# Performance work log

Measured on AMD Instinct MI355X. Metric: run time of the kernel, lower is better.

Reference implementation:

```python
import jax, jax.numpy as jnp
import numpy as np

B, L, D = 2, 1024, 1024
H = 16
NL = 2
DFF = 4 * D
EPS = 1e-5
W_SCALE = 0.02


def rmsnorm(x, w):
    # x * rsqrt(mean(x^2, -1) + eps) * w   (computed in fp32 as in the torch code)
    xf = x.astype(jnp.float32)
    n = xf * jax.lax.rsqrt(jnp.mean(xf * xf, axis=-1, keepdims=True) + EPS)
    return n.astype(x.dtype) * w


def setup_inputs() -> dict:
    key = jax.random.key(0)
    ks = jax.random.split(key, 10)
    x = jax.random.normal(ks[0], (B, L, D), dtype=jnp.float32)
    # torch nn.Linear weight layout: [out_features, in_features]; y = x @ W.T + b
    qw = jax.random.normal(ks[1], (NL, D, D), dtype=jnp.float32) * W_SCALE
    kw = jax.random.normal(ks[2], (NL, D, D), dtype=jnp.float32) * W_SCALE
    vw = jax.random.normal(ks[3], (NL, D, D), dtype=jnp.float32) * W_SCALE
    ow = jax.random.normal(ks[4], (NL, D, D), dtype=jnp.float32) * W_SCALE
    pn_w = jnp.ones((NL, D), dtype=jnp.float32)
    ln_w = jnp.ones((NL, D), dtype=jnp.float32)
    fc_w = jax.random.normal(ks[5], (NL, DFF, D), dtype=jnp.float32) * W_SCALE
    fc2_w = jax.random.normal(ks[6], (NL, D, DFF), dtype=jnp.float32) * W_SCALE
    fc2_b = jnp.zeros((NL, D), dtype=jnp.float32)
    return {"x": x, "qw": qw, "kw": kw, "vw": vw, "ow": ow,
            "pn_w": pn_w, "ln_w": ln_w, "fc_w": fc_w, "fc2_w": fc2_w, "fc2_b": fc2_b}


def reference(x, qw, kw, vw, ow, pn_w, ln_w, fc_w, fc2_w, fc2_b):
    d = D // H
    for i in range(NL):
        # --- LinearAttention block (dropout=0 -> identity) ---
        h = rmsnorm(x, pn_w[i])                                   # [B,L,D]
        Q = (h @ qw[i].T).reshape(B, L, H, d)
        K = (h @ kw[i].T).reshape(B, L, H, d)
        V = (h @ vw[i].T).reshape(B, L, H, d)
        # outer-product state per position, cumulated over L (causal linear attn)
        W = jnp.einsum('blhd,blhe->blhde', K, V)                  # [B,L,H,d,d]
        W = jnp.cumsum(W, axis=1)
        a = jnp.einsum('blhd,blhde->blhe', Q, W).reshape(B, L, D)
        x = x + a @ ow[i].T
        # --- MLP block ---
        m = rmsnorm(x, ln_w[i])
        f = jax.nn.gelu(m @ fc_w[i].T, approximate=False)         # torch nn.GELU default = exact
        x = x + f @ fc2_w[i].T + fc2_b[i]
    return x
```

## Files before the change

kernel.cpp:

```cpp
#include <hip/hip_runtime.h>

#define BB 2
#define LL 1024
#define DD 1024
#define HH 16
#define HD 64
#define DFFN 4096
#define MM (BB*LL)
#define QS 3072

using u16 = unsigned short;
typedef __bf16 bf16x8 __attribute__((ext_vector_type(8)));
typedef float f32x4 __attribute__((ext_vector_type(4)));

__device__ __forceinline__ float b2f(u16 u) {
  union { unsigned int i; float f; } v; v.i = ((unsigned int)u) << 16; return v.f;
}
__device__ __forceinline__ u16 f2b(float f) {
  union { float f; unsigned int i; } v; v.f = f;
  unsigned int x = v.i;
  return (u16)((x + 0x7fffu + ((x >> 16) & 1u)) >> 16);
}
__device__ __forceinline__ float gelu_exact(float x) {
  return 0.5f * x * (1.0f + erff(x * 0.70710678118654752f));
}
__device__ __forceinline__ void gl2lds16(const void* g, void* l) {
  __builtin_amdgcn_global_load_lds((const __attribute__((address_space(1))) void*)g,
                                   (__attribute__((address_space(3))) void*)l, 16, 0, 0);
}

template<int N>
__device__ __forceinline__ void s_wait_vm() {
  if constexpr (N == 0)       asm volatile("s_waitcnt vmcnt(0)" ::: "memory");
  else if constexpr (N == 3)  asm volatile("s_waitcnt vmcnt(3)" ::: "memory");
  else if constexpr (N == 6)  asm volatile("s_waitcnt vmcnt(6)" ::: "memory");
  else if constexpr (N == 12) asm volatile("s_waitcnt vmcnt(12)" ::: "memory");
  __builtin_amdgcn_sched_barrier(0);
}

__device__ __forceinline__ void xcd_remap(int& bx, int& by, int& bz) {
  const int gx = gridDim.x, gy = gridDim.y;
  const int nb = gx * gy * gridDim.z;
  int b = blockIdx.x + gx * (blockIdx.y + gy * blockIdx.z);
  if ((nb & 127) == 0) {
    const int xcd = b & 7, seq = b >> 3;
    b = (((seq >> 4) << 3) + xcd) * 16 + (seq & 15);
  }
  bx = b % gx; const int rest = b / gx;
  by = rest % gy; bz = rest / gy;
}

__global__ __launch_bounds__(256) void castw_kernel(const float* __restrict__ in,
                                                    u16* __restrict__ out, int n8) {
  int i = blockIdx.x * 256 + threadIdx.x;
  if (i >= n8) return;
  const float4 a = reinterpret_cast<const float4*>(in)[2 * i];
  const float4 b = reinterpret_cast<const float4*>(in)[2 * i + 1];
  uint4 o;
  o.x = (unsigned)f2b(a.x) | ((unsigned)f2b(a.y) << 16);
  o.y = (unsigned)f2b(a.z) | ((unsigned)f2b(a.w) << 16);
  o.z = (unsigned)f2b(b.x) | ((unsigned)f2b(b.y) << 16);
  o.w = (unsigned)f2b(b.z) | ((unsigned)f2b(b.w) << 16);
  reinterpret_cast<uint4*>(out)[i] = o;
}
__global__ __launch_bounds__(256) void castw3_kernel(const float* __restrict__ s0,
                                                     const float* __restrict__ s1,
                                                     const float* __restrict__ s2,
                                                     u16* __restrict__ out, int n8) {
  int i = blockIdx.x * 256 + threadIdx.x;
  if (i >= n8) return;
  const float* in = (blockIdx.y == 0) ? s0 : (blockIdx.y == 1) ? s1 : s2;
  u16* dst = out + (size_t)blockIdx.y * n8 * 8;
  const float4 a = reinterpret_cast<const float4*>(in)[2 * i];
  const float4 b = reinterpret_cast<const float4*>(in)[2 * i + 1];
  uint4 o;
  o.x = (unsigned)f2b(a.x) | ((unsigned)f2b(a.y) << 16);
  o.y = (unsigned)f2b(a.z) | ((unsigned)f2b(a.w) << 16);
  o.z = (unsigned)f2b(b.x) | ((unsigned)f2b(b.y) << 16);
  o.w = (unsigned)f2b(b.z) | ((unsigned)f2b(b.w) << 16);
  reinterpret_cast<uint4*>(dst)[i] = o;
}

__global__ __launch_bounds__(256) void rmsnorm_kernel(const float* __restrict__ x,
                                                      const float* __restrict__ w,
                                                      u16* __restrict__ out) {
  const int row = blockIdx.x, t = threadIdx.x;
  const float4 v = reinterpret_cast<const float4*>(x + (size_t)row * DD)[t];
  float ss = v.x*v.x + v.y*v.y + v.z*v.z + v.w*v.w;
  #pragma unroll
  for (int o = 32; o > 0; o >>= 1) ss += __shfl_down(ss, o);
  __shared__ float red[4];
  if ((t & 63) == 0) red[t >> 6] = ss;
  __syncthreads();
  const float inv = rsqrtf((red[0] + red[1] + red[2] + red[3]) * (1.0f / DD) + 1e-5f);
  const float4 wv = reinterpret_cast<const float4*>(w)[t];
  ushort4 o;
  o.x = f2b(v.x * inv * wv.x);
  o.y = f2b(v.y * inv * wv.y);
  o.z = f2b(v.z * inv * wv.z);
  o.w = f2b(v.w * inv * wv.w);
  reinterpret_cast<ushort4*>(out + (size_t)row * DD)[t] = o;
}

__global__ __launch_bounds__(256) void reduce_add_kernel(float* __restrict__ co,
                                                         const float* __restrict__ P0,
                                                         const float* __restrict__ P1) {
  const int i = blockIdx.x * 256 + threadIdx.x;
  constexpr int HALF = (MM / 2) * DD / 4;
  const float4 p = (i < HALF) ? reinterpret_cast<const float4*>(P0)[i]
                              : reinterpret_cast<const float4*>(P1)[i - HALF];
  float4 v = reinterpret_cast<float4*>(co)[i];
  v.x += p.x; v.y += p.y; v.z += p.z; v.w += p.w;
  reinterpret_cast<float4*>(co)[i] = v;
}

template<int ROWS, int NT>
__device__ __forceinline__ void dma32(const u16* __restrict__ g, int r0, int K, int kt,
                                      int t, u16* lds) {
  #pragma unroll
  for (int i = 0; i < ROWS * 4 / NT; i++) {
    const int c = i * NT + t;
    const int row = (c & 7) | ((c >> 5) << 3);
    const int kc = (c >> 3) & 3;
    gl2lds16(g + (size_t)(r0 + row) * K + kt + kc * 8, &lds[c * 8]);
  }
}
__device__ __forceinline__ const bf16x8* lds_frag(const u16* base, int r, int fq) {
  const int p = (r & 7) | (fq << 3) | ((r >> 3) << 5);
  return reinterpret_cast<const bf16x8*>(&base[p * 8]);
}

#define MFMA_BF16 __builtin_amdgcn_mfma_f32_16x16x32_bf16

template<int BM, int BN>
__device__ __forceinline__ void gemm_pipe(const u16* __restrict__ A,
                                          const u16* __restrict__ Wb,
                                          int K, int k0, int nt, int m0, int n0,
                                          u16* As, u16* Bs, int t,
                                          int wm, int wn, int fr, int fq,
                                          f32x4 acc[4][4]) {
  constexpr int NT = (BM / 64) * (BN / 64) * 64;
  constexpr int LT = (BM + BN) * 4 / NT;
  #pragma unroll
  for (int s = 0; s < 3; ++s) {
    dma32<BM, NT>(A, m0, K, k0 + s * 32, t, As + s * BM * 32);
    dma32<BN, NT>(Wb, n0, K, k0 + s * 32, t, Bs + s * BN * 32);
  }
  s_wait_vm<2 * LT>();
  __builtin_amdgcn_s_barrier();
  int pb = 0;
  for (int tt = 0; tt < nt; ++tt) {
    const u16* Asb = As + pb * BM * 32;
    const u16* Bsb = Bs + pb * BN * 32;
    const int p3 = (pb + 3) & 3;
    const bool st = (tt + 3 < nt);
    bf16x8 a0 = *lds_frag(Asb, wm + 0 * 16 + fr, fq);
    bf16x8 a1 = *lds_frag(Asb, wm + 1 * 16 + fr, fq);
    bf16x8 b0 = *lds_frag(Bsb, wn + 0 * 16 + fr, fq);
    bf16x8 b1 = *lds_frag(Bsb, wn + 1 * 16 + fr, fq);
    bf16x8 b2 = *lds_frag(Bsb, wn + 2 * 16 + fr, fq);
    bf16x8 b3 = *lds_frag(Bsb, wn + 3 * 16 + fr, fq);
    if (st) dma32<BM, NT>(A, m0, K, k0 + (tt + 3) * 32, t, As + p3 * BM * 32);
    __builtin_amdgcn_sched_barrier(0);
    __builtin_amdgcn_s_barrier();
    asm volatile("s_waitcnt lgkmcnt(0)" ::: "memory");
    __builtin_amdgcn_sched_barrier(0);
    __builtin_amdgcn_s_setprio(1);
    acc[0][0] = MFMA_BF16(a0, b0, acc[0][0], 0, 0, 0);
    acc[0][1] = MFMA_BF16(a0, b1, acc[0][1], 0, 0, 0);
    acc[0][2] = MFMA_BF16(a0, b2, acc[0][2], 0, 0, 0);
    acc[0][3] = MFMA_BF16(a0, b3, acc[0][3], 0, 0, 0);
    acc[1][0] = MFMA_BF16(a1, b0, acc[1][0], 0, 0, 0);
    acc[1][1] = MFMA_BF16(a1, b1, acc[1][1], 0, 0, 0);
    acc[1][2] = MFMA_BF16(a1, b2, acc[1][2], 0, 0, 0);
    acc[1][3] = MFMA_BF16(a1, b3, acc[1][3], 0, 0, 0);
    __builtin_amdgcn_s_setprio(0);
    __builtin_amdgcn_sched_barrier(0);
    __builtin_amdgcn_s_barrier();
    bf16x8 a2 = *lds_frag(Asb, wm + 2 * 16 + fr, fq);
    bf16x8 a3 = *lds_frag(Asb, wm + 3 * 16 + fr, fq);
    if (st) dma32<BN, NT>(Wb, n0, K, k0 + (tt + 3) * 32, t, Bs + p3 * BN * 32);
    __builtin_amdgcn_sched_barrier(0);
    __builtin_amdgcn_s_barrier();
    asm volatile("s_waitcnt lgkmcnt(0)" ::: "memory");
    __builtin_amdgcn_sched_barrier(0);
    __builtin_amdgcn_s_setprio(1);
    acc[2][0] = MFMA_BF16(a2, b0, acc[2][0], 0, 0, 0);
    acc[2][1] = MFMA_BF16(a2, b1, acc[2][1], 0, 0, 0);
    acc[2][2] = MFMA_BF16(a2, b2, acc[2][2], 0, 0, 0);
    acc[2][3] = MFMA_BF16(a2, b3, acc[2][3], 0, 0, 0);
    acc[3][0] = MFMA_BF16(a3, b0, acc[3][0], 0, 0, 0);
    acc[3][1] = MFMA_BF16(a3, b1, acc[3][1], 0, 0, 0);
    acc[3][2] = MFMA_BF16(a3, b2, acc[3][2], 0, 0, 0);
    acc[3][3] = MFMA_BF16(a3, b3, acc[3][3], 0, 0, 0);
    __builtin_amdgcn_s_setprio(0);
    __builtin_amdgcn_sched_barrier(0);
    if (tt + 1 < nt) {
      const int rem = nt - 2 - tt;
      if (rem >= 2)      s_wait_vm<2 * LT>();
      else if (rem == 1) s_wait_vm<LT>();
      else               s_wait_vm<0>();
      __builtin_amdgcn_s_barrier();
    }
    pb = (pb + 1) & 3;
  }
}

template<int BM, int BN, int ACT>
__global__ __launch_bounds__((BM/64)*(BN/64)*64)
void mfma_gemm(const u16* __restrict__ A, const u16* __restrict__ Wb,
               u16* __restrict__ Cb, int N, int K) {
  constexpr int WCOLS = BN / 64;
  __shared__ u16 As[4 * BM * 32];
  __shared__ u16 Bs[4 * BN * 32];
  int bx, by, bz;
  xcd_remap(bx, by, bz);
  const int t = threadIdx.x;
  const int lane = t & 63, w = t >> 6;
  const int wm = (w / WCOLS) * 64, wn = (w % WCOLS) * 64;
  const int m0 = by * BM, n0 = bx * BN;
  const int fr = lane & 15, fq = lane >> 4;

  f32x4 acc[4][4] = {};
  gemm_pipe<BM, BN>(A, Wb, K, 0, K / 32, m0, n0, As, Bs, t, wm, wn, fr, fq, acc);

  #pragma unroll
  for (int i = 0; i < 4; i++)
    #pragma unroll
    for (int j = 0; j < 4; j++)
      #pragma unroll
      for (int r = 0; r < 4; r++) {
        const int row = m0 + wm + i * 16 + fq * 4 + r;
        const int col = n0 + wn + j * 16 + fr;
        float val = acc[i][j][r];
        if (ACT == 1) val = gelu_exact(val);
        Cb[(size_t)row * N + col] = f2b(val);
      }
}

template<int BM, int BN>
__global__ __launch_bounds__((BM/64)*(BN/64)*64)
void mfma_gemm_fo(const u16* __restrict__ A, const u16* __restrict__ Wb,
                  const float* __restrict__ resid, const float* __restrict__ bias,
                  float* __restrict__ Co, float* __restrict__ P0, float* __restrict__ P1,
                  int N, int K, int Kc) {
  constexpr int WCOLS = BN / 64;
  __shared__ u16 As[4 * BM * 32];
  __shared__ u16 Bs[4 * BN * 32];
  int bx, by, bz;
  xcd_remap(bx, by, bz);
  const int t = threadIdx.x;
  const int lane = t & 63, w = t >> 6;
  const int wm = (w / WCOLS) * 64, wn = (w % WCOLS) * 64;
  const int m0 = by * BM, n0 = bx * BN;
  const int fr = lane & 15, fq = lane >> 4;
  const int k0 = bz * Kc;

  f32x4 acc[4][4] = {};
  gemm_pipe<BM, BN>(A, Wb, K, k0, Kc / 32, m0, n0, As, Bs, t, wm, wn, fr, fq, acc);

  if (bz == 0) {
    #pragma unroll
    for (int j = 0; j < 4; j++) {
      const int col = n0 + wn + j * 16 + fr;
      const float bj = (bias != nullptr) ? bias[col] : 0.0f;
      #pragma unroll
      for (int i = 0; i < 4; i++)
        #pragma unroll
        for (int r = 0; r < 4; r++) {
          const int row = m0 + wm + i * 16 + fq * 4 + r;
          const size_t idx = (size_t)row * N + col;
          Co[idx] = resid[idx] + bj + acc[i][j][r];
        }
    }
  } else {
    #pragma unroll
    for (int j = 0; j < 4; j++) {
      const int col = n0 + wn + j * 16 + fr;
      #pragma unroll
      for (int i = 0; i < 4; i++)
        #pragma unroll
        for (int r = 0; r < 4; r++) {
          const int row = m0 + wm + i * 16 + fq * 4 + r;
          float* P = (row < MM / 2) ? P0 : P1;
          P[(size_t)(row & (MM / 2 - 1)) * N + col] = acc[i][j][r];
        }
    }
  }
}

__global__ __launch_bounds__(256) void kv_trans(const u16* __restrict__ QKV,
                                                u16* __restrict__ Kt, u16* __restrict__ Vt) {
  __shared__ u16 T[64][72];
  const int tile = blockIdx.x;
  const int h2 = blockIdx.y;
  const int b = blockIdx.z;
  const int h = h2 & 15, which = h2 >> 4;
  const int t = threadIdx.x;
  const int pos = t >> 2, d0 = (t & 3) * 16;
  const u16* src = QKV + ((size_t)(b * LL) + tile * 64 + pos) * QS + 1024 + which * 1024 + h * HD + d0;
  union { uint4 u[2]; u16 s[16]; } pk;
  pk.u[0] = reinterpret_cast<const uint4*>(src)[0];
  pk.u[1] = reinterpret_cast<const uint4*>(src)[1];
  #pragma unroll
  for (int j = 0; j < 16; j++) T[d0 + j][pos] = pk.s[j];
  __syncthreads();
  const int d = t >> 2, p0 = (t & 3) * 16;
  u16* dst = (which ? Vt : Kt) + ((size_t)(b * HH + h) * HD + d) * LL + tile * 64 + p0;
  union { uint4 u[2]; u16 s[16]; } ok;
  #pragma unroll
  for (int j = 0; j < 16; j++) ok.s[j] = T[d][p0 + j];
  reinterpret_cast<uint4*>(dst)[0] = ok.u[0];
  reinterpret_cast<uint4*>(dst)[1] = ok.u[1];
}

__global__ __launch_bounds__(256) void attn_phase1(const u16* __restrict__ QKV,
                                                   const u16* __restrict__ Kt,
                                                   const u16* __restrict__ Vt,
                                                   u16* __restrict__ Oa,
                                                   u16* __restrict__ Slt) {
  __shared__ u16 Ss[4][16][64];
  const int tile = blockIdx.x, h = blockIdx.y, b = blockIdx.z;
  const int t = threadIdx.x, lane = t & 63, w = t >> 6;
  const int fr = lane & 15, fq = lane >> 4;
  const size_t tok0 = (size_t)(b * LL + tile * 64);
  const size_t bh = (size_t)(b * HH + h);
  const u16* Qb  = QKV + tok0 * QS + h * HD;
  const u16* Kb  = Qb + 1024;
  const u16* Ktb = Kt + bh * (HD * LL) + tile * 64;
  const u16* Vtb = Vt + bh * (HD * LL) + tile * 64;

  bf16x8 aq[2], bk[4][2];
  #pragma unroll
  for (int kh = 0; kh < 2; kh++)
    aq[kh] = *reinterpret_cast<const bf16x8*>(Qb + (size_t)(16*w + fr) * QS + kh*32 + fq*8);
  #pragma unroll
  for (int n4 = 0; n4 < 4; n4++)
    #pragma unroll
    for (int kh = 0; kh < 2; kh++)
      bk[n4][kh] = *reinterpret_cast<const bf16x8*>(Kb + (size_t)(16*n4 + fr) * QS + kh*32 + fq*8);
  f32x4 sacc[4] = {};
  #pragma unroll
  for (int n4 = 0; n4 < 4; n4++) {
    sacc[n4] = MFMA_BF16(aq[0], bk[n4][0], sacc[n4], 0, 0, 0);
    sacc[n4] = MFMA_BF16(aq[1], bk[n4][1], sacc[n4], 0, 0, 0);
  }
  #pragma unroll
  for (int n4 = 0; n4 < 4; n4++)
    #pragma unroll
    for (int r = 0; r < 4; r++) {
      const bool keep = (16*w + 4*fq + r) >= (16*n4 + fr);
      Ss[w][4*fq + r][16*n4 + fr] = keep ? f2b(sacc[n4][r]) : (u16)0;
    }
  __syncthreads();

  bf16x8 va[2], kt[4][2];
  #pragma unroll
  for (int kh = 0; kh < 2; kh++)
    va[kh] = *reinterpret_cast<const bf16x8*>(Vtb + (size_t)(16*w + fr) * LL + kh*32 + fq*8);
  #pragma unroll
  for (int n4 = 0; n4 < 4; n4++)
    #pragma unroll
    for (int kh = 0; kh < 2; kh++)
      kt[n4][kh] = *reinterpret_cast<const bf16x8*>(Ktb + (size_t)(16*n4 + fr) * LL + kh*32 + fq*8);
  f32x4 lacc[4] = {};
  #pragma unroll
  for (int n4 = 0; n4 < 4; n4++) {
    lacc[n4] = MFMA_BF16(va[0], kt[n4][0], lacc[n4], 0, 0, 0);
    lacc[n4] = MFMA_BF16(va[1], kt[n4][1], lacc[n4], 0, 0, 0);
  }
  u16* So = Slt + (bh * 16 + tile) * 4096;
  #pragma unroll
  for (int n4 = 0; n4 < 4; n4++)
    #pragma unroll
    for (int r = 0; r < 4; r++)
      So[(size_t)(16*w + 4*fq + r) * 64 + 16*n4 + fr] = f2b(lacc[n4][r]);

  bf16x8 sa[2], vb[4][2];
  #pragma unroll
  for (int kh = 0; kh < 2; kh++)
    sa[kh] = *reinterpret_cast<const bf16x8*>(&Ss[w][fr][kh*32 + fq*8]);
  #pragma unroll
  for (int n4 = 0; n4 < 4; n4++)
    #pragma unroll
    for (int kh = 0; kh < 2; kh++)
      vb[n4][kh] = *reinterpret_cast<const bf16x8*>(Vtb + (size_t)(16*n4 + fr) * LL + kh*32 + fq*8);
  f32x4 oacc[4] = {};
  #pragma unroll
  for (int n4 = 0; n4 < 4; n4++) {
    oacc[n4] = MFMA_BF16(sa[0], vb[n4][0], oacc[n4], 0, 0, 0);
    oacc[n4] = MFMA_BF16(sa[1], vb[n4][1], oacc[n4], 0, 0, 0);
  }
  u16* Ob = Oa + (tok0 + 16*w) * DD + h * HD;
  #pragma unroll
  for (int n4 = 0; n4 < 4; n4++)
    #pragma unroll
    for (int r = 0; r < 4; r++)
      Ob[(size_t)(4*fq + r) * DD + 16*n4 + fr] = f2b(oacc[n4][r]);
}

__global__ __launch_bounds__(256) void attn_phase2(const u16* __restrict__ Slt,
                                                   u16* __restrict__ Wc) {
  const int rg = blockIdx.x, h = blockIdx.y, b = blockIdx.z;
  const size_t base = ((size_t)((b * HH + h) * 16)) * 4096 + rg * 512 + threadIdx.x * 2;
  float r0 = 0.f, r1 = 0.f;
  for (int tl = 0; tl < 16; tl++) {
    const size_t p = base + (size_t)tl * 4096;
    const unsigned d = *reinterpret_cast<const unsigned*>(Slt + p);
    *reinterpret_cast<unsigned*>(Wc + p) = (unsigned)f2b(r0) | ((unsigned)f2b(r1) << 16);
    r0 += b2f((u16)(d & 0xffff));
    r1 += b2f((u16)(d >> 16));
  }
}

__global__ __launch_bounds__(256) void attn_phase3(const u16* __restrict__ QKV,
                                                   const u16* __restrict__ Wc,
                                                   u16* __restrict__ Oa) {
  const int tile = blockIdx.x, h = blockIdx.y, b = blockIdx.z;
  const int t = threadIdx.x, lane = t & 63, w = t >> 6;
  const int fr = lane & 15, fq = lane >> 4;
  const size_t tok0 = (size_t)(b * LL + tile * 64);
  const size_t bh = (size_t)(b * HH + h);
  const u16* Qb = QKV + tok0 * QS + h * HD;
  const u16* Wb = Wc + (bh * 16 + tile) * 4096;

  bf16x8 aq[2], wb[4][2];
  #pragma unroll
  for (int kh = 0; kh < 2; kh++)
    aq[kh] = *reinterpret_cast<const bf16x8*>(Qb + (size_t)(16*w + fr) * QS + kh*32 + fq*8);
  #pragma unroll
  for (int n4 = 0; n4 < 4; n4++)
    #pragma unroll
    for (int kh = 0; kh < 2; kh++)
      wb[n4][kh] = *reinterpret_cast<const bf16x8*>(Wb + (size_t)(16*n4 + fr) * 64 + kh*32 + fq*8);
  f32x4 oacc[4] = {};
  #pragma unroll
  for (int n4 = 0; n4 < 4; n4++) {
    oacc[n4] = MFMA_BF16(aq[0], wb[n4][0], oacc[n4], 0, 0, 0);
    oacc[n4] = MFMA_BF16(aq[1], wb[n4][1], oacc[n4], 0, 0, 0);
  }
  u16* Ob = Oa + (tok0 + 16*w) * DD + h * HD;
  #pragma unroll
  for (int n4 = 0; n4 < 4; n4++)
    #pragma unroll
    for (int r = 0; r < 4; r++) {
      const size_t idx = (size_t)(4*fq + r) * DD + 16*n4 + fr;
      Ob[idx] = f2b(b2f(Ob[idx]) + oacc[n4][r]);
    }
}

extern "C" void kernel_launch(void* const* d_in, const int* in_sizes, int n_in,
                              void* d_out, int out_size, void* d_ws, size_t ws_size,
                              hipStream_t stream) {
  const float* x_in = (const float*)d_in[0];
  const float* qw   = (const float*)d_in[1];
  const float* kw   = (const float*)d_in[2];
  const float* vw   = (const float*)d_in[3];
  const float* ow   = (const float*)d_in[4];
  const float* pn   = (const float*)d_in[5];
  const float* ln   = (const float*)d_in[6];
  const float* fcw  = (const float*)d_in[7];
  const float* fc2w = (const float*)d_in[8];
  const float* fc2b = (const float*)d_in[9];

  char* ws = (char*)d_ws;
  u16* wbuf = (u16*)ws;
  u16* slt  = (u16*)ws;
  u16* wcum = (u16*)(ws + (size_t)(4 << 20));
  u16* h    = (u16*)(ws + (size_t)(8 << 20));
  u16* qkv  = (u16*)(ws + (size_t)(12 << 20));
  u16* f    = (u16*)(ws + (size_t)(12 << 20));
  u16* vt   = (u16*)(ws + (size_t)(24 << 20));
  u16* kt   = (u16*)(ws + (size_t)(28 << 20));
  float* p0 = (float*)(ws + (size_t)(8 << 20));
  float* p1 = (float*)(ws + (size_t)(28 << 20));
  float* xf = (float*)d_out;

  const int n8D = DD * DD / 8;
  const int n8F = DFFN * DD / 8;

  for (int i = 0; i < 2; i++) {
    const float* qwi  = qw   + (size_t)i * DD * DD;
    const float* kwi  = kw   + (size_t)i * DD * DD;
    const float* vwi  = vw   + (size_t)i * DD * DD;
    const float* owi  = ow   + (size_t)i * DD * DD;
    const float* fcwi = fcw  + (size_t)i * DFFN * DD;
    const float* f2wi = fc2w + (size_t)i * DD * DFFN;
    const float* src  = (i == 0) ? x_in : xf;

    rmsnorm_kernel<<<MM, 256, 0, stream>>>(src, pn + i * DD, h);
    castw3_kernel<<<dim3(n8D / 256, 3), 256, 0, stream>>>(qwi, kwi, vwi, wbuf, n8D);
    mfma_gemm<256, 128, 0><<<dim3(QS / 128, MM / 256), 512, 0, stream>>>(
        h, wbuf, qkv, QS, DD);
    kv_trans<<<dim3(16, 32, BB), 256, 0, stream>>>(qkv, kt, vt);
    attn_phase1<<<dim3(16, HH, BB), 256, 0, stream>>>(qkv, kt, vt, h, slt);
    attn_phase2<<<dim3(8, HH, BB), 256, 0, stream>>>(slt, wcum);
    attn_phase3<<<dim3(16, HH, BB), 256, 0, stream>>>(qkv, wcum, h);
    castw_kernel<<<n8D / 256, 256, 0, stream>>>(owi, wbuf, n8D);
    mfma_gemm_fo<128, 64><<<dim3(DD / 64, MM / 128, 1), 128, 0, stream>>>(
        h, wbuf, src, nullptr, xf, p0, p1, DD, DD, DD);
    rmsnorm_kernel<<<MM, 256, 0, stream>>>(xf, ln + i * DD, h);
    castw_kernel<<<n8F / 256, 256, 0, stream>>>(fcwi, wbuf, n8F);
    mfma_gemm<256, 128, 1><<<dim3(DFFN / 128, MM / 256), 512, 0, stream>>>(
        h, wbuf, f, DFFN, DD);
    castw_kernel<<<n8F / 256, 256, 0, stream>>>(f2wi, wbuf, n8F);
    float* co = (i == 1) ? (float*)d_out : xf;
    mfma_gemm_fo<128, 64><<<dim3(DD / 64, MM / 128, 2), 128, 0, stream>>>(
        f, wbuf, xf, fc2b + i * DD, co, p0, p1, DD, DFFN, DFFN / 2);
    reduce_add_kernel<<<MM * DD / 4 / 256, 256, 0, stream>>>(co, p0, p1);
  }
}
```

Measured before the change: 571.1 us.

## Replace pipelined GEMM with simple single-buffer loop, retile, split-K out-proj

Removes the 4-stage LDS prefetch pipeline, with its manual vmcnt/lgkmcnt waits and barriers, and uses a plain load, sync, MFMA, sync loop over single-buffered LDS. All GEMMs now use 128x128 tiles with 256 threads. The output projection gains a 2-way split-K with a separate reduction kernel. This cuts LDS use and code complexity, but global loads no longer overlap with MFMA work, so memory latency is exposed on every K step.

```diff
diff --git a/kernel.cpp b/kernel.cpp
--- a/kernel.cpp
+++ b/kernel.cpp
@@ -27,15 +27,6 @@
 __device__ __forceinline__ void gl2lds16(const void* g, void* l) {
   __builtin_amdgcn_global_load_lds((const __attribute__((address_space(1))) void*)g,
                                    (__attribute__((address_space(3))) void*)l, 16, 0, 0);
-}
-
-template<int N>
-__device__ __forceinline__ void s_wait_vm() {
-  if constexpr (N == 0)       asm volatile("s_waitcnt vmcnt(0)" ::: "memory");
-  else if constexpr (N == 3)  asm volatile("s_waitcnt vmcnt(3)" ::: "memory");
-  else if constexpr (N == 6)  asm volatile("s_waitcnt vmcnt(6)" ::: "memory");
-  else if constexpr (N == 12) asm volatile("s_waitcnt vmcnt(12)" ::: "memory");
-  __builtin_amdgcn_sched_barrier(0);
 }
 
 __device__ __forceinline__ void xcd_remap(int& bx, int& by, int& bz) {
@@ -132,77 +123,34 @@
 
 #define MFMA_BF16 __builtin_amdgcn_mfma_f32_16x16x32_bf16
 
+__device__ __forceinline__ void mfma_tile32(const u16* Asb, const u16* Bsb,
+                                            int wm, int wn, int fr, int fq, f32x4 acc[4][4]) {
+  bf16x8 af[4], bfv[4];
+  #pragma unroll
+  for (int i = 0; i < 4; i++) af[i] = *lds_frag(Asb, wm + i * 16 + fr, fq);
+  #pragma unroll
+  for (int j = 0; j < 4; j++) bfv[j] = *lds_frag(Bsb, wn + j * 16 + fr, fq);
+  #pragma unroll
+  for (int i = 0; i < 4; i++)
+    #pragma unroll
+    for (int j = 0; j < 4; j++)
+      acc[i][j] = MFMA_BF16(af[i], bfv[j], acc[i][j], 0, 0, 0);
+}
+
 template<int BM, int BN>
-__device__ __forceinline__ void gemm_pipe(const u16* __restrict__ A,
+__device__ __forceinline__ void gemm_loop(const u16* __restrict__ A,
                                           const u16* __restrict__ Wb,
-                                          int K, int k0, int nt, int m0, int n0,
+                                          int K, int k0, int kend, int m0, int n0,
                                           u16* As, u16* Bs, int t,
                                           int wm, int wn, int fr, int fq,
                                           f32x4 acc[4][4]) {
   constexpr int NT = (BM / 64) * (BN / 64) * 64;
-  constexpr int LT = (BM + BN) * 4 / NT;
-  #pragma unroll
-  for (int s = 0; s < 3; ++s) {
-    dma32<BM, NT>(A, m0, K, k0 + s * 32, t, As + s * BM * 32);
-    dma32<BN, NT>(Wb, n0, K, k0 + s * 32, t, Bs + s * BN * 32);
-  }
-  s_wait_vm<2 * LT>();
-  __builtin_amdgcn_s_barrier();
-  int pb = 0;
-  for (int tt = 0; tt < nt; ++tt) {
-    const u16* Asb = As + pb * BM * 32;
-    const u16* Bsb = Bs + pb * BN * 32;
-    const int p3 = (pb + 3) & 3;
-    const bool st = (tt + 3 < nt);
-    bf16x8 a0 = *lds_frag(Asb, wm + 0 * 16 + fr, fq);
-    bf16x8 a1 = *lds_frag(Asb, wm + 1 * 16 + fr, fq);
-    bf16x8 b0 = *lds_frag(Bsb, wn + 0 * 16 + fr, fq);
-    bf16x8 b1 = *lds_frag(Bsb, wn + 1 * 16 + fr, fq);
-    bf16x8 b2 = *lds_frag(Bsb, wn + 2 * 16 + fr, fq);
-    bf16x8 b3 = *lds_frag(Bsb, wn + 3 * 16 + fr, fq);
-    if (st) dma32<BM, NT>(A, m0, K, k0 + (tt + 3) * 32, t, As + p3 * BM * 32);
-    __builtin_amdgcn_sched_barrier(0);
-    __builtin_amdgcn_s_barrier();
-    asm volatile("s_waitcnt lgkmcnt(0)" ::: "memory");
-    __builtin_amdgcn_sched_barrier(0);
-    __builtin_amdgcn_s_setprio(1);
-    acc[0][0] = MFMA_BF16(a0, b0, acc[0][0], 0, 0, 0);
-    acc[0][1] = MFMA_BF16(a0, b1, acc[0][1], 0, 0, 0);
-    acc[0][2] = MFMA_BF16(a0, b2, acc[0][2], 0, 0, 0);
-    acc[0][3] = MFMA_BF16(a0, b3, acc[0][3], 0, 0, 0);
-    acc[1][0] = MFMA_BF16(a1, b0, acc[1][0], 0, 0, 0);
-    acc[1][1] = MFMA_BF16(a1, b1, acc[1][1], 0, 0, 0);
-    acc[1][2] = MFMA_BF16(a1, b2, acc[1][2], 0, 0, 0);
-    acc[1][3] = MFMA_BF16(a1, b3, acc[1][3], 0, 0, 0);
-    __builtin_amdgcn_s_setprio(0);
-    __builtin_amdgcn_sched_barrier(0);
-    __builtin_amdgcn_s_barrier();
-    bf16x8 a2 = *lds_frag(Asb, wm + 2 * 16 + fr, fq);
-    bf16x8 a3 = *lds_frag(Asb, wm + 3 * 16 + fr, fq);
-    if (st) dma32<BN, NT>(Wb, n0, K, k0 + (tt + 3) * 32, t, Bs + p3 * BN * 32);
-    __builtin_amdgcn_sched_barrier(0);
-    __builtin_amdgcn_s_barrier();
-    asm volatile("s_waitcnt lgkmcnt(0)" ::: "memory");
-    __builtin_amdgcn_sched_barrier(0);
-    __builtin_amdgcn_s_setprio(1);
-    acc[2][0] = MFMA_BF16(a2, b0, acc[2][0], 0, 0, 0);
-    acc[2][1] = MFMA_BF16(a2, b1, acc[2][1], 0, 0, 0);
-    acc[2][2] = MFMA_BF16(a2, b2, acc[2][2], 0, 0, 0);
-    acc[2][3] = MFMA_BF16(a2, b3, acc[2][3], 0, 0, 0);
-    acc[3][0] = MFMA_BF16(a3, b0, acc[3][0], 0, 0, 0);
-    acc[3][1] = MFMA_BF16(a3, b1, acc[3][1], 0, 0, 0);
-    acc[3][2] = MFMA_BF16(a3, b2, acc[3][2], 0, 0, 0);
-    acc[3][3] = MFMA_BF16(a3, b3, acc[3][3], 0, 0, 0);
-    __builtin_amdgcn_s_setprio(0);
-    __builtin_amdgcn_sched_barrier(0);
-    if (tt + 1 < nt) {
-      const int rem = nt - 2 - tt;
-      if (rem >= 2)      s_wait_vm<2 * LT>();
-      else if (rem == 1) s_wait_vm<LT>();
-      else               s_wait_vm<0>();
-      __builtin_amdgcn_s_barrier();
-    }
-    pb = (pb + 1) & 3;
+  for (int kt = k0; kt < kend; kt += 32) {
+    dma32<BM, NT>(A, m0, K, kt, t, As);
+    dma32<BN, NT>(Wb, n0, K, kt, t, Bs);
+    __syncthreads();
+    mfma_tile32(As, Bs, wm, wn, fr, fq, acc);
+    __syncthreads();
   }
 }
 
@@ -211,8 +159,8 @@
 void mfma_gemm(const u16* __restrict__ A, const u16* __restrict__ Wb,
                u16* __restrict__ Cb, int N, int K) {
   constexpr int WCOLS = BN / 64;
-  __shared__ u16 As[4 * BM * 32];
-  __shared__ u16 Bs[4 * BN * 32];
+  __shared__ u16 As[BM * 32];
+  __shared__ u16 Bs[BN * 32];
   int bx, by, bz;
   xcd_remap(bx, by, bz);
   const int t = threadIdx.x;
@@ -222,7 +170,7 @@
   const int fr = lane & 15, fq = lane >> 4;
 
   f32x4 acc[4][4] = {};
-  gemm_pipe<BM, BN>(A, Wb, K, 0, K / 32, m0, n0, As, Bs, t, wm, wn, fr, fq, acc);
+  gemm_loop<BM, BN>(A, Wb, K, 0, K, m0, n0, As, Bs, t, wm, wn, fr, fq, acc);
 
   #pragma unroll
   for (int i = 0; i < 4; i++)
@@ -245,8 +193,8 @@
                   float* __restrict__ Co, float* __restrict__ P0, float* __restrict__ P1,
                   int N, int K, int Kc) {
   constexpr int WCOLS = BN / 64;
-  __shared__ u16 As[4 * BM * 32];
-  __shared__ u16 Bs[4 * BN * 32];
+  __shared__ u16 As[BM * 32];
+  __shared__ u16 Bs[BN * 32];
   int bx, by, bz;
   xcd_remap(bx, by, bz);
   const int t = threadIdx.x;
@@ -257,7 +205,7 @@
   const int k0 = bz * Kc;
 
   f32x4 acc[4][4] = {};
-  gemm_pipe<BM, BN>(A, Wb, K, k0, Kc / 32, m0, n0, As, Bs, t, wm, wn, fr, fq, acc);
+  gemm_loop<BM, BN>(A, Wb, K, k0, k0 + Kc, m0, n0, As, Bs, t, wm, wn, fr, fq, acc);
 
   if (bz == 0) {
     #pragma unroll
@@ -474,10 +422,12 @@
   u16* kt   = (u16*)(ws + (size_t)(28 << 20));
   float* p0 = (float*)(ws + (size_t)(8 << 20));
   float* p1 = (float*)(ws + (size_t)(28 << 20));
+  float* pq = (float*)(ws + (size_t)(12 << 20));
   float* xf = (float*)d_out;
 
   const int n8D = DD * DD / 8;
   const int n8F = DFFN * DD / 8;
+  constexpr int HALFF = (MM / 2) * DD;
 
   for (int i = 0; i < 2; i++) {
     const float* qwi  = qw   + (size_t)i * DD * DD;
@@ -490,22 +440,23 @@
 
     rmsnorm_kernel<<<MM, 256, 0, stream>>>(src, pn + i * DD, h);
     castw3_kernel<<<dim3(n8D / 256, 3), 256, 0, stream>>>(qwi, kwi, vwi, wbuf, n8D);
-    mfma_gemm<256, 128, 0><<<dim3(QS / 128, MM / 256), 512, 0, stream>>>(
+    mfma_gemm<128, 128, 0><<<dim3(QS / 128, MM / 128), 256, 0, stream>>>(
         h, wbuf, qkv, QS, DD);
     kv_trans<<<dim3(16, 32, BB), 256, 0, stream>>>(qkv, kt, vt);
     attn_phase1<<<dim3(16, HH, BB), 256, 0, stream>>>(qkv, kt, vt, h, slt);
     attn_phase2<<<dim3(8, HH, BB), 256, 0, stream>>>(slt, wcum);
     attn_phase3<<<dim3(16, HH, BB), 256, 0, stream>>>(qkv, wcum, h);
     castw_kernel<<<n8D / 256, 256, 0, stream>>>(owi, wbuf, n8D);
-    mfma_gemm_fo<128, 64><<<dim3(DD / 64, MM / 128, 1), 128, 0, stream>>>(
-        h, wbuf, src, nullptr, xf, p0, p1, DD, DD, DD);
+    mfma_gemm_fo<128, 128><<<dim3(DD / 128, MM / 128, 2), 256, 0, stream>>>(
+        h, wbuf, src, nullptr, xf, pq, pq + HALFF, DD, DD, DD / 2);
+    reduce_add_kernel<<<MM * DD / 4 / 256, 256, 0, stream>>>(xf, pq, pq + HALFF);
     rmsnorm_kernel<<<MM, 256, 0, stream>>>(xf, ln + i * DD, h);
     castw_kernel<<<n8F / 256, 256, 0, stream>>>(fcwi, wbuf, n8F);
-    mfma_gemm<256, 128, 1><<<dim3(DFFN / 128, MM / 256), 512, 0, stream>>>(
+    mfma_gemm<128, 128, 1><<<dim3(DFFN / 128, MM / 128), 256, 0, stream>>>(
         h, wbuf, f, DFFN, DD);
     castw_kernel<<<n8F / 256, 256, 0, stream>>>(f2wi, wbuf, n8F);
     float* co = (i == 1) ? (float*)d_out : xf;
-    mfma_gemm_fo<128, 64><<<dim3(DD / 64, MM / 128, 2), 128, 0, stream>>>(
+    mfma_gemm_fo<128, 128><<<dim3(DD / 128, MM / 128, 2), 256, 0, stream>>>(
         f, wbuf, xf, fc2b + i * DD, co, p0, p1, DD, DFFN, DFFN / 2);
     reduce_add_kernel<<<MM * DD / 4 / 256, 256, 0, stream>>>(co, p0, p1);
   }
```

After: 608.3 us. 1.07x slower.
